# Performance work log

Hardware: AMD Instinct MI355X
Metric: run time of the kernel (lower is better)

The kernel has to match this reference:

```python
import jax, jax.numpy as jnp
import numpy as np
from jax import lax

B, C, T, S = 32, 122, 500, 13
WID, EMB, PROJ = 80, 8, 1024
HID = 768  # (H=1)*(W=96)*(E=8) after CNN
EPS = 1e-5
DN = ('NCHW', 'OIHW', 'NCHW')


def setup_inputs() -> dict:
    key = jax.random.key(0)
    ks = jax.random.split(key, 24)
    f32 = jnp.float32
    def n(k, shape, scale):
        return (jax.random.normal(k, shape, dtype=f32) * scale).astype(f32)
    return {
        'x': jax.random.normal(ks[0], (B, C, T), dtype=f32),
        'subject_ids': jax.random.randint(ks[1], (B,), 0, S, dtype=jnp.int32),
        'W_sub': n(ks[2], (S, T, T), 0.04),      # nn.Linear(500,500) weight per subject
        'b_sub': n(ks[3], (S, T), 0.02),
        'conv1_w': n(ks[4], (WID, 1, 1, 5), 0.3),
        'conv1_b': n(ks[5], (WID,), 0.02),
        'bn1_g': 1.0 + n(ks[6], (WID,), 0.1),
        'bn1_b': n(ks[7], (WID,), 0.1),
        'bn1_m': n(ks[8], (WID,), 0.1),
        'bn1_v': 0.5 + jax.random.uniform(ks[9], (WID,), dtype=f32),
        'conv2_w': n(ks[10], (WID, WID, C, 1), 0.01),
        'conv2_b': n(ks[11], (WID,), 0.02),
        'bn2_g': 1.0 + n(ks[12], (WID,), 0.1),
        'bn2_b': n(ks[13], (WID,), 0.1),
        'bn2_m': n(ks[14], (WID,), 0.1),
        'bn2_v': 0.5 + jax.random.uniform(ks[15], (WID,), dtype=f32),
        'proj_w': n(ks[16], (EMB, WID, 1, 1), 0.1),
        'proj_b': n(ks[17], (EMB,), 0.02),
        'mlp1_w': n(ks[18], (PROJ, HID), 0.03),
        'mlp1_b': n(ks[19], (PROJ,), 0.02),
        'mlp2_w': n(ks[20], (PROJ, PROJ), 0.03),
        'mlp2_b': n(ks[21], (PROJ,), 0.02),
        'ln_g': 1.0 + n(ks[22], (PROJ,), 0.05),
        'ln_b': n(ks[23], (PROJ,), 0.05),
    }


def _bn(h, g, b, m, v):
    # eval-mode BatchNorm2d over channel axis 1
    scale = (g / jnp.sqrt(v + EPS))[None, :, None, None]
    shift = (b - m * g / jnp.sqrt(v + EPS))[None, :, None, None]
    return h * scale + shift


def _forward(x, subject_ids, W_sub, b_sub, conv1_w, conv1_b, bn1_g, bn1_b, bn1_m, bn1_v,
             conv2_w, conv2_b, bn2_g, bn2_b, bn2_m, bn2_v, proj_w, proj_b,
             mlp1_w, mlp1_b, mlp2_w, mlp2_b, ln_g, ln_b):
    # --- per-subject routing: gather each sample's Linear(500,500) and apply ---
    Wg = W_sub[subject_ids]                       # [B,T,T] (out,in)
    bg = b_sub[subject_ids]                       # [B,T]
    out = jnp.einsum('bcs,bts->bct', x, Wg) + bg[:, None, :]
    # --- spatio-temporal CNN (eval mode: dropout = identity) ---
    h = out[:, None, :, :]                        # [B,1,C,T]
    h = lax.conv_general_dilated(h, conv1_w, (1, 1), 'VALID', dimension_numbers=DN)
    h = h + conv1_b[None, :, None, None]          # [B,80,122,496]
    h = lax.reduce_window(h, 0.0, lax.add, (1, 1, 1, 17), (1, 1, 1, 5), 'VALID') / 17.0  # [B,80,122,96]
    h = jax.nn.elu(_bn(h, bn1_g, bn1_b, bn1_m, bn1_v))
    h = lax.conv_general_dilated(h, conv2_w, (1, 1), 'VALID', dimension_numbers=DN)
    h = h + conv2_b[None, :, None, None]          # [B,80,1,96]
    h = jax.nn.elu(_bn(h, bn2_g, bn2_b, bn2_m, bn2_v))
    h = lax.conv_general_dilated(h, proj_w, (1, 1), 'VALID', dimension_numbers=DN)
    h = h + proj_b[None, :, None, None]           # [B,8,1,96]
    z = jnp.transpose(h, (0, 2, 3, 1)).reshape(h.shape[0], -1)  # [B,768]
    # --- MLP projector: Linear -> Residual(GELU+Linear) -> LayerNorm ---
    z1 = z @ mlp1_w.T + mlp1_b                    # [B,1024]
    r = jax.nn.gelu(z1, approximate=False) @ mlp2_w.T + mlp2_b
    y = z1 + r
    mu = jnp.mean(y, axis=-1, keepdims=True)
    var = jnp.var(y, axis=-1, keepdims=True)
    return (y - mu) / jnp.sqrt(var + EPS) * ln_g + ln_b


def reference(x, subject_ids, W_sub, b_sub, conv1_w, conv1_b, bn1_g, bn1_b, bn1_m, bn1_v,
              conv2_w, conv2_b, bn2_g, bn2_b, bn2_m, bn2_v, proj_w, proj_b,
              mlp1_w, mlp1_b, mlp2_w, mlp2_b, ln_g, ln_b):
    return _forward(x, subject_ids, W_sub, b_sub, conv1_w, conv1_b, bn1_g, bn1_b, bn1_m, bn1_v,
                    conv2_w, conv2_b, bn2_g, bn2_b, bn2_m, bn2_v, proj_w, proj_b,
                    mlp1_w, mlp1_b, mlp2_w, mlp2_b, ln_g, ln_b)
```

## Files before the change

### kernel.cpp

```cpp
#include <hip/hip_runtime.h>
#include <math.h>

#define BB 32
#define CC 122
#define TT 500
#define SS 13
#define WID 80
#define EMB 8
#define PROJ 1024
#define HID 768
#define TP 96
#define EPSF 1e-5f
#define KP 9760
#define KSPLIT 16

typedef float f32x4 __attribute__((ext_vector_type(4)));
typedef __bf16 bf16x8 __attribute__((ext_vector_type(8)));
typedef unsigned short u16x8 __attribute__((ext_vector_type(8)));
union BF8 { u16x8 u; bf16x8 b; };

__device__ __forceinline__ unsigned short f2bf(float f) {
    union { float f; unsigned u; } v; v.f = f;
    unsigned r = v.u + 0x7FFFu + ((v.u >> 16) & 1u);
    return (unsigned short)(r >> 16);
}

__device__ __forceinline__ float eluf(float x) {
    return x > 0.f ? x : __expf(x) - 1.f;
}

#define OFF_E    ((size_t)0)
#define OFF_XB   ((size_t)1952000)
#define OFF_W2P  ((size_t)4704512)
#define OFF_PART ((size_t)20086272)
#define OFF_Z    ((size_t)24018432)
#define OFF_Z1   ((size_t)24030720)
#define OFF_G    ((size_t)24063488)
#define OFF_Y    ((size_t)24079872)
#define OFF_W1B  ((size_t)24112640)
#define OFF_W2B  ((size_t)24505856)
#define OFF_WCB  ((size_t)25030144)
#define OFF_B1F  ((size_t)25031424)
#define OFF_SC2  ((size_t)25031504)
#define OFF_SH2  ((size_t)25031584)

#define NPK_X  (2097152)
#define NPK_M1 (786432)
#define NPK_M2 (1048576)
#define NPK_LIN (NPK_X + NPK_M1 + NPK_M2)

__global__ __launch_bounds__(256) void k_pack(const float* __restrict__ x,
                                              const float* __restrict__ conv2_w,
                                              const float* __restrict__ mlp1_w,
                                              const float* __restrict__ mlp2_w,
                                              const float* __restrict__ conv1_w, const float* __restrict__ conv1_b,
                                              const float* __restrict__ g1, const float* __restrict__ b1,
                                              const float* __restrict__ m1, const float* __restrict__ v1,
                                              const float* __restrict__ conv2_b, const float* __restrict__ g2,
                                              const float* __restrict__ b2, const float* __restrict__ m2,
                                              const float* __restrict__ v2,
                                              unsigned short* __restrict__ xb,
                                              unsigned short* __restrict__ w2p,
                                              unsigned short* __restrict__ w1b,
                                              unsigned short* __restrict__ w2b,
                                              unsigned short* __restrict__ wcb, float* __restrict__ bias1f,
                                              float* __restrict__ scale2, float* __restrict__ shift2f) {
    __shared__ unsigned short lt[WID][124];
    int bid = blockIdx.x, tid = threadIdx.x;
    if (bid < WID) {
        if (bid == 0 && tid < WID) {
            int o = tid;
            float s1 = g1[o] * rsqrtf(v1[o] + EPSF);
            float sh1 = b1[o] - m1[o] * s1;
            #pragma unroll
            for (int d = 0; d < 21; d++) {
                int klo = d - 16; if (klo < 0) klo = 0;
                int khi = d;      if (khi > 4) khi = 4;
                float acc = 0.f;
                for (int k = klo; k <= khi; k++) acc += conv1_w[o*5 + k];
                wcb[o*32 + d] = f2bf(acc * s1 * (1.f/17.f));
            }
            #pragma unroll
            for (int d = 21; d < 32; d++) wcb[o*32 + d] = 0;
            bias1f[o] = conv1_b[o] * s1 + sh1;
            float s2 = g2[o] * rsqrtf(v2[o] + EPSF);
            scale2[o] = s2;
            shift2f[o] = conv2_b[o] * s2 + (b2[o] - m2[o] * s2);
        }
        int o = bid;
        const float* src = conv2_w + (size_t)o * (WID * CC);
        for (int i = tid; i < WID * CC; i += 256) {
            int op = i / CC, c = i - op * CC;
            lt[op][c] = f2bf(src[i]);
        }
        __syncthreads();
        unsigned short* dst = w2p + (size_t)o * KP;
        for (int j = tid; j < KP / 8; j += 256) {
            int k0 = j * 8;
            union { unsigned short h[8]; uint4 q; } pk;
            #pragma unroll
            for (int u = 0; u < 8; u++) {
                int k = k0 + u;
                pk.h[u] = lt[k % WID][k / WID];
            }
            *(uint4*)(dst + k0) = pk.q;
        }
        return;
    }
    size_t idx = (size_t)(bid - WID) * 256 + tid;
    if (idx >= (size_t)NPK_LIN) return;
    if (idx < NPK_X) {
        int u = (int)(idx & 7);
        size_t j = idx >> 3;
        int l  = (int)(j & 63); j >>= 6;
        int kk = (int)(j & 15); j >>= 4;
        int sp = (int)(j & 7);
        int b  = (int)(j >> 3);
        int c  = sp * 16 + (l & 15);
        int s  = kk * 32 + (l >> 4) * 8 + u;
        float v = (c < CC && s < TT) ? x[((size_t)b * CC + c) * TT + s] : 0.f;
        xb[idx] = f2bf(v);
    } else if (idx < NPK_X + NPK_M1) {
        size_t j = idx - NPK_X;
        w1b[j] = f2bf(mlp1_w[j]);
    } else {
        size_t j = idx - NPK_X - NPK_M1;
        w2b[j] = f2bf(mlp2_w[j]);
    }
}

__global__ __launch_bounds__(256) void k_einsum(const unsigned short* __restrict__ xb,
                                                const float* __restrict__ W_sub,
                                                const int* __restrict__ sid,
                                                const float* __restrict__ b_sub,
                                                unsigned short* __restrict__ oute) {
    __shared__ unsigned short bt[32 * 520];
    int t0 = blockIdx.x * 32, b = blockIdx.y;
    int s = sid[b];
    int tid = threadIdx.x, w = tid >> 6, lr = tid & 15, lg = (tid >> 4) & 3;
    {
        const float* src = W_sub + (size_t)s * (TT * TT);
        for (int i = tid; i < 2048; i += 256) {
            int row = i >> 6;
            int c0  = (i & 63) << 3;
            int rt  = t0 + row;
            union { unsigned short h[8]; uint4 q; } pk;
            if (rt < TT && c0 + 8 <= TT) {
                const float* p = src + (size_t)rt * TT + c0;
                float4 v0 = *(const float4*)p;
                float4 v1 = *(const float4*)(p + 4);
                pk.h[0] = f2bf(v0.x); pk.h[1] = f2bf(v0.y);
                pk.h[2] = f2bf(v0.z); pk.h[3] = f2bf(v0.w);
                pk.h[4] = f2bf(v1.x); pk.h[5] = f2bf(v1.y);
                pk.h[6] = f2bf(v1.z); pk.h[7] = f2bf(v1.w);
            } else {
                const float* p = src + (size_t)rt * TT;
                #pragma unroll
                for (int j = 0; j < 8; j++)
                    pk.h[j] = (rt < TT && c0 + j < TT) ? f2bf(p[c0 + j]) : (unsigned short)0;
            }
            *(uint4*)(&bt[row * 520 + c0]) = pk.q;
        }
    }
    __syncthreads();
    const unsigned short* A0 = xb + ((size_t)(b * 8 + w * 2) * 16) * 512 + (size_t)(tid & 63) * 8;
    f32x4 acc[2][2] = {};
    for (int kk = 0; kk < 16; kk++) {
        BF8 a0, a1;
        a0.u = *(const u16x8*)(A0 + kk * 512);
        a1.u = *(const u16x8*)(A0 + 16 * 512 + kk * 512);
        #pragma unroll
        for (int nt = 0; nt < 2; nt++) {
            BF8 bf; bf.u = *(const u16x8*)(bt + (nt * 16 + lr) * 520 + kk * 32 + 8 * lg);
            acc[0][nt] = __builtin_amdgcn_mfma_f32_16x16x32_bf16(a0.b, bf.b, acc[0][nt], 0, 0, 0);
            acc[1][nt] = __builtin_amdgcn_mfma_f32_16x16x32_bf16(a1.b, bf.b, acc[1][nt], 0, 0, 0);
        }
    }
    const float* bg = b_sub + (size_t)s * TT;
    #pragma unroll
    for (int nt = 0; nt < 2; nt++) {
        int t = t0 + nt * 16 + lr;
        if (t < TT) {
            float bias = bg[t];
            #pragma unroll
            for (int mt = 0; mt < 2; mt++) {
                int crow = w * 32 + mt * 16 + 4 * lg;
                #pragma unroll
                for (int r = 0; r < 4; r++) {
                    int c = crow + r;
                    if (c < CC) oute[((size_t)b * CC + c) * TT + t] = f2bf(acc[mt][nt][r] + bias);
                }
            }
        }
    }
}

__global__ __launch_bounds__(384) void k_fc(const unsigned short* __restrict__ oute,
                                            const unsigned short* __restrict__ wcb,
                                            const float* __restrict__ b1f,
                                            const unsigned short* __restrict__ w2p,
                                            float* __restrict__ part) {
    __shared__ unsigned short e2[2][512];
    __shared__ unsigned short pt[96][164];
    __shared__ unsigned short aw[WID][168];
    int chunk = blockIdx.x, b = blockIdx.y;
    int tid = threadIdx.x, w = tid >> 6, l = tid & 63, lr = l & 15, lg = l >> 4;
    BF8 af[5]; float4 bf4[5];
    #pragma unroll
    for (int ot = 0; ot < 5; ot++) {
        af[ot].u = *(const u16x8*)(wcb + (ot * 16 + lr) * 32 + 8 * lg);
        bf4[ot] = *(const float4*)(b1f + ot * 16 + 4 * lg);
    }
    f32x4 acc2[5] = {};
    for (int ci = 0; ci < 4; ci++) {
        int cp = chunk * 4 + ci;
        bool live = cp < 61;
        __syncthreads();
        if (live) {
            if (tid < 250) {
                int cc = tid / 125, i = tid % 125;
                ((uint2*)e2[cc])[i] = ((const uint2*)(oute + ((size_t)b * CC + cp * 2 + cc) * TT))[i];
            }
            if (tid >= 232 && tid < 256) {
                int j = tid - 232; int cc = j / 12, i = 500 + (j % 12);
                e2[cc][i] = 0;
            }
            const unsigned short* wsrc = w2p + (size_t)cp * 160;
            for (int i = tid; i < WID * 20; i += 384) {
                int o = i / 20, c8 = i - o * 20;
                *(u16x8*)(&aw[o][c8 * 8]) = *(const u16x8*)(wsrc + (size_t)o * KP + c8 * 8);
            }
        }
        __syncthreads();
        if (live) {
            #pragma unroll
            for (int cc = 0; cc < 2; cc++) {
                int t = w * 16 + lr;
                const unsigned short* ew = e2[cc] + 5 * t + 8 * lg;
                BF8 bfr;
                #pragma unroll
                for (int j = 0; j < 8; j++) bfr.u[j] = ew[j];
                f32x4 fa[5] = {};
                #pragma unroll
                for (int ot = 0; ot < 5; ot++)
                    fa[ot] = __builtin_amdgcn_mfma_f32_16x16x32_bf16(af[ot].b, bfr.b, fa[ot], 0, 0, 0);
                #pragma unroll
                for (int ot = 0; ot < 5; ot++) {
                    union { unsigned short s[4]; uint2 v; } pk;
                    #pragma unroll
                    for (int r = 0; r < 4; r++) pk.s[r] = f2bf(eluf(fa[ot][r] + bf4[ot][r]));
                    *(uint2*)&pt[t][cc * 80 + ot * 16 + 4 * lg] = pk.v;
                }
            }
        }
        __syncthreads();
        if (live) {
            #pragma unroll
            for (int kl = 0; kl < 5; kl++) {
                BF8 bf; bf.u = *(const u16x8*)(&pt[w * 16 + lr][kl * 32 + lg * 8]);
                #pragma unroll
                for (int mt = 0; mt < 5; mt++) {
                    BF8 a; a.u = *(const u16x8*)(&aw[mt * 16 + lr][kl * 32 + lg * 8]);
                    acc2[mt] = __builtin_amdgcn_mfma_f32_16x16x32_bf16(a.b, bf.b, acc2[mt], 0, 0, 0);
                }
            }
        }
    }
    float* pp = part + ((size_t)(chunk * BB + b) * WID) * TP;
    int t = w * 16 + lr;
    #pragma unroll
    for (int mt = 0; mt < 5; mt++) {
        int ob = mt * 16 + 4 * lg;
        #pragma unroll
        for (int r = 0; r < 4; r++)
            pp[(size_t)(ob + r) * TP + t] = acc2[mt][r];
    }
}

__global__ __launch_bounds__(256) void k_redproj(const float* __restrict__ part,
                                                 const float* __restrict__ scale2,
                                                 const float* __restrict__ shift2f,
                                                 const float* __restrict__ pw,
                                                 const float* __restrict__ pb,
                                                 unsigned short* __restrict__ zbf) {
    __shared__ float ly[WID * 12];
    __shared__ float lw[EMB * WID];
    int tq = blockIdx.x, b = blockIdx.y;
    int tid = threadIdx.x;
    int t0 = tq * 12;
    for (int i = tid; i < EMB * WID; i += 256) lw[i] = pw[i];
    if (tid < 240) {
        int o = tid / 3, q = tid % 3;
        const float* pbase = part + (size_t)b * (WID * TP) + o * TP + t0 + 4 * q;
        float4 a = {0.f, 0.f, 0.f, 0.f};
        #pragma unroll
        for (int ks = 0; ks < KSPLIT; ks++) {
            float4 v = *(const float4*)(pbase + (size_t)ks * (BB * WID * TP));
            a.x += v.x; a.y += v.y; a.z += v.z; a.w += v.w;
        }
        float sc = scale2[o], sh = shift2f[o];
        ly[o * 12 + 4 * q + 0] = eluf(a.x * sc + sh);
        ly[o * 12 + 4 * q + 1] = eluf(a.y * sc + sh);
        ly[o * 12 + 4 * q + 2] = eluf(a.z * sc + sh);
        ly[o * 12 + 4 * q + 3] = eluf(a.w * sc + sh);
    }
    __syncthreads();
    if (tid < 12 * EMB) {
        int e = tid & 7, tl = tid >> 3;
        float acc = pb[e];
        #pragma unroll 10
        for (int o = 0; o < WID; o++) acc = fmaf(ly[o * 12 + tl], lw[e * WID + o], acc);
        zbf[(size_t)b * HID + (t0 + tl) * EMB + e] = f2bf(acc);
    }
}

__global__ __launch_bounds__(256) void k_mlp1(const unsigned short* __restrict__ zbf,
                                              const unsigned short* __restrict__ w1b,
                                              const float* __restrict__ bias,
                                              float* __restrict__ z1,
                                              unsigned short* __restrict__ gbf) {
    __shared__ float accb[4][64][4];
    int cu = blockIdx.x >> 1, rh = blockIdx.x & 1;
    int tid = threadIdx.x, w = tid >> 6, l = tid & 63, lr = l & 15, lg = l >> 4;
    int pcol = cu * 16 + lr;
    const unsigned short* wr = w1b + (size_t)pcol * HID + w * 192 + 8 * lg;
    const unsigned short* za = zbf + (size_t)(rh * 16 + lr) * HID + w * 192 + 8 * lg;
    f32x4 acc = {};
    #pragma unroll
    for (int kb = 0; kb < 192; kb += 32) {
        BF8 bf; bf.u = *(const u16x8*)(wr + kb);
        BF8 a;  a.u  = *(const u16x8*)(za + kb);
        acc = __builtin_amdgcn_mfma_f32_16x16x32_bf16(a.b, bf.b, acc, 0, 0, 0);
    }
    #pragma unroll
    for (int r = 0; r < 4; r++) accb[w][l][r] = acc[r];
    __syncthreads();
    if (w == 0) {
        float bs = bias[pcol];
        #pragma unroll
        for (int r = 0; r < 4; r++) {
            int row = rh * 16 + 4 * lg + r;
            float v = bs;
            #pragma unroll
            for (int q = 0; q < 4; q++) v += accb[q][l][r];
            z1[(size_t)row * PROJ + pcol] = v;
            gbf[(size_t)row * PROJ + pcol] = f2bf(0.5f * v * (1.f + erff(v * 0.70710678118654752f)));
        }
    }
}

__global__ __launch_bounds__(256) void k_mlp2(const unsigned short* __restrict__ gbf,
                                              const float* __restrict__ z1,
                                              const unsigned short* __restrict__ w2b,
                                              const float* __restrict__ bias,
                                              float* __restrict__ y) {
    __shared__ float accb[4][64][4];
    int cu = blockIdx.x >> 1, rh = blockIdx.x & 1;
    int tid = threadIdx.x, w = tid >> 6, l = tid & 63, lr = l & 15, lg = l >> 4;
    int pc = cu * 16 + lr;
    const unsigned short* wr = w2b + (size_t)pc * PROJ + w * 256 + 8 * lg;
    const unsigned short* ga = gbf + (size_t)(rh * 16 + lr) * PROJ + w * 256 + 8 * lg;
    f32x4 acc = {};
    #pragma unroll
    for (int kb = 0; kb < 256; kb += 32) {
        BF8 bf; bf.u = *(const u16x8*)(wr + kb);
        BF8 a;  a.u  = *(const u16x8*)(ga + kb);
        acc = __builtin_amdgcn_mfma_f32_16x16x32_bf16(a.b, bf.b, acc, 0, 0, 0);
    }
    #pragma unroll
    for (int r = 0; r < 4; r++) accb[w][l][r] = acc[r];
    __syncthreads();
    if (w == 0) {
        float bs = bias[pc];
        #pragma unroll
        for (int r = 0; r < 4; r++) {
            int row = rh * 16 + 4 * lg + r;
            float v = bs + z1[(size_t)row * PROJ + pc];
            #pragma unroll
            for (int q = 0; q < 4; q++) v += accb[q][l][r];
            y[(size_t)row * PROJ + pc] = v;
        }
    }
}

__global__ __launch_bounds__(256) void k_ln(const float* __restrict__ y,
                                            const float* __restrict__ lg,
                                            const float* __restrict__ lb,
                                            float* __restrict__ out) {
    int b = blockIdx.x, tid = threadIdx.x;
    const float4* yr = (const float4*)(y + (size_t)b * PROJ);
    float4 v = yr[tid];
    float s  = v.x + v.y + v.z + v.w;
    float sq = v.x*v.x + v.y*v.y + v.z*v.z + v.w*v.w;
    #pragma unroll
    for (int off = 32; off > 0; off >>= 1) {
        s  += __shfl_down(s, off);
        sq += __shfl_down(sq, off);
    }
    __shared__ float ss[4], ssq[4];
    int wv = tid >> 6, lane = tid & 63;
    if (lane == 0) { ss[wv] = s; ssq[wv] = sq; }
    __syncthreads();
    __shared__ float smu, sinv;
    if (tid == 0) {
        float Sm = ss[0] + ss[1] + ss[2] + ss[3];
        float Sq = ssq[0] + ssq[1] + ssq[2] + ssq[3];
        float mu = Sm * (1.f / PROJ);
        float var = Sq * (1.f / PROJ) - mu * mu;
        smu = mu;
        sinv = rsqrtf(var + EPSF);
    }
    __syncthreads();
    float mu = smu, inv = sinv;
    float4 g4 = ((const float4*)lg)[tid];
    float4 b4 = ((const float4*)lb)[tid];
    float4 o4;
    o4.x = (v.x - mu) * inv * g4.x + b4.x;
    o4.y = (v.y - mu) * inv * g4.y + b4.y;
    o4.z = (v.z - mu) * inv * g4.z + b4.z;
    o4.w = (v.w - mu) * inv * g4.w + b4.w;
    ((float4*)(out + (size_t)b * PROJ))[tid] = o4;
}

extern "C" void kernel_launch(void* const* d_in, const int* in_sizes, int n_in,
                              void* d_out, int out_size, void* d_ws, size_t ws_size,
                              hipStream_t stream) {
    const float* x        = (const float*)d_in[0];
    const int*   sid      = (const int*)  d_in[1];
    const float* W_sub    = (const float*)d_in[2];
    const float* b_sub    = (const float*)d_in[3];
    const float* conv1_w  = (const float*)d_in[4];
    const float* conv1_b  = (const float*)d_in[5];
    const float* bn1_g    = (const float*)d_in[6];
    const float* bn1_b    = (const float*)d_in[7];
    const float* bn1_m    = (const float*)d_in[8];
    const float* bn1_v    = (const float*)d_in[9];
    const float* conv2_w  = (const float*)d_in[10];
    const float* conv2_b  = (const float*)d_in[11];
    const float* bn2_g    = (const float*)d_in[12];
    const float* bn2_b    = (const float*)d_in[13];
    const float* bn2_m    = (const float*)d_in[14];
    const float* bn2_v    = (const float*)d_in[15];
    const float* proj_w   = (const float*)d_in[16];
    const float* proj_b   = (const float*)d_in[17];
    const float* mlp1_w   = (const float*)d_in[18];
    const float* mlp1_b   = (const float*)d_in[19];
    const float* mlp2_w   = (const float*)d_in[20];
    const float* mlp2_b   = (const float*)d_in[21];
    const float* ln_g     = (const float*)d_in[22];
    const float* ln_b     = (const float*)d_in[23];
    float* out = (float*)d_out;
    float* ws  = (float*)d_ws;

    unsigned short* ws_e   = (unsigned short*)(ws + OFF_E);
    unsigned short* ws_xb  = (unsigned short*)(ws + OFF_XB);
    unsigned short* ws_w2p = (unsigned short*)(ws + OFF_W2P);
    float* ws_part = ws + OFF_PART;
    unsigned short* ws_zbf = (unsigned short*)(ws + OFF_Z);
    float* ws_z1   = ws + OFF_Z1;
    unsigned short* ws_gbf = (unsigned short*)(ws + OFF_G);
    float* ws_y    = ws + OFF_Y;
    unsigned short* ws_w1b = (unsigned short*)(ws + OFF_W1B);
    unsigned short* ws_w2b = (unsigned short*)(ws + OFF_W2B);
    unsigned short* ws_wcb = (unsigned short*)(ws + OFF_WCB);
    float* ws_b1f  = ws + OFF_B1F;
    float* ws_sc2  = ws + OFF_SC2;
    float* ws_sh2  = ws + OFF_SH2;

    hipLaunchKernelGGL(k_pack, dim3(WID + (NPK_LIN + 255) / 256), dim3(256), 0, stream,
                       x, conv2_w, mlp1_w, mlp2_w,
                       conv1_w, conv1_b, bn1_g, bn1_b, bn1_m, bn1_v,
                       conv2_b, bn2_g, bn2_b, bn2_m, bn2_v,
                       ws_xb, ws_w2p, ws_w1b, ws_w2b,
                       ws_wcb, ws_b1f, ws_sc2, ws_sh2);

    hipLaunchKernelGGL(k_einsum, dim3(16, BB), dim3(256), 0, stream,
                       ws_xb, W_sub, sid, b_sub, ws_e);

    hipLaunchKernelGGL(k_fc, dim3(KSPLIT, BB), dim3(384), 0, stream,
                       ws_e, ws_wcb, ws_b1f, ws_w2p, ws_part);

    hipLaunchKernelGGL(k_redproj, dim3(8, BB), dim3(256), 0, stream,
                       ws_part, ws_sc2, ws_sh2, proj_w, proj_b, ws_zbf);

    hipLaunchKernelGGL(k_mlp1, dim3(128), dim3(256), 0, stream,
                       ws_zbf, ws_w1b, mlp1_b, ws_z1, ws_gbf);

    hipLaunchKernelGGL(k_mlp2, dim3(128), dim3(256), 0, stream,
                       ws_gbf, ws_z1, ws_w2b, mlp2_b, ws_y);

    hipLaunchKernelGGL(k_ln, dim3(BB), dim3(256), 0, stream,
                       ws_y, ln_g, ln_b, out);
}
```

Measured before the change: 193.0 us.

## Move weight conversion into einsum launch to overlap with einsum work

Pulls the mlp1/mlp2 bf16 conversion and the conv2 weight repacking out of k_pack and runs them as extra blocks appended to the k_einsum grid. Those blocks need no einsum output, so they can execute alongside the einsum tiles instead of lengthening the serial pack kernel. The mlp copy is also vectorised to 8 elements per thread with float4 loads. The cost is a larger, heterogeneous einsum grid whose copy blocks compete with the einsum tiles for compute units and bandwidth.

```diff
diff --git a/kernel.cpp b/kernel.cpp
--- a/kernel.cpp
+++ b/kernel.cpp
@@ -47,12 +47,11 @@
 #define NPK_X  (2097152)
 #define NPK_M1 (786432)
 #define NPK_M2 (1048576)
-#define NPK_LIN (NPK_X + NPK_M1 + NPK_M2)
+#define M1M2_CHUNKS ((NPK_M1 + NPK_M2) / 8)
+#define NCPY 256
+#define NEIN (512 + NCPY + WID)
 
 __global__ __launch_bounds__(256) void k_pack(const float* __restrict__ x,
-                                              const float* __restrict__ conv2_w,
-                                              const float* __restrict__ mlp1_w,
-                                              const float* __restrict__ mlp2_w,
                                               const float* __restrict__ conv1_w, const float* __restrict__ conv1_b,
                                               const float* __restrict__ g1, const float* __restrict__ b1,
                                               const float* __restrict__ m1, const float* __restrict__ v1,
@@ -60,16 +59,11 @@
                                               const float* __restrict__ b2, const float* __restrict__ m2,
                                               const float* __restrict__ v2,
                                               unsigned short* __restrict__ xb,
-                                              unsigned short* __restrict__ w2p,
-                                              unsigned short* __restrict__ w1b,
-                                              unsigned short* __restrict__ w2b,
                                               unsigned short* __restrict__ wcb, float* __restrict__ bias1f,
                                               float* __restrict__ scale2, float* __restrict__ shift2f) {
-    __shared__ unsigned short lt[WID][124];
-    int bid = blockIdx.x, tid = threadIdx.x;
-    if (bid < WID) {
-        if (bid == 0 && tid < WID) {
-            int o = tid;
+    if (blockIdx.x == 0) {
+        int o = threadIdx.x;
+        if (o < WID) {
             float s1 = g1[o] * rsqrtf(v1[o] + EPSF);
             float sh1 = b1[o] - m1[o] * s1;
             #pragma unroll
@@ -87,57 +81,78 @@
             scale2[o] = s2;
             shift2f[o] = conv2_b[o] * s2 + (b2[o] - m2[o] * s2);
         }
-        int o = bid;
-        const float* src = conv2_w + (size_t)o * (WID * CC);
-        for (int i = tid; i < WID * CC; i += 256) {
-            int op = i / CC, c = i - op * CC;
-            lt[op][c] = f2bf(src[i]);
-        }
-        __syncthreads();
-        unsigned short* dst = w2p + (size_t)o * KP;
-        for (int j = tid; j < KP / 8; j += 256) {
-            int k0 = j * 8;
-            union { unsigned short h[8]; uint4 q; } pk;
-            #pragma unroll
-            for (int u = 0; u < 8; u++) {
-                int k = k0 + u;
-                pk.h[u] = lt[k % WID][k / WID];
-            }
-            *(uint4*)(dst + k0) = pk.q;
-        }
-        return;
-    }
-    size_t idx = (size_t)(bid - WID) * 256 + tid;
-    if (idx >= (size_t)NPK_LIN) return;
-    if (idx < NPK_X) {
-        int u = (int)(idx & 7);
-        size_t j = idx >> 3;
-        int l  = (int)(j & 63); j >>= 6;
-        int kk = (int)(j & 15); j >>= 4;
-        int sp = (int)(j & 7);
-        int b  = (int)(j >> 3);
-        int c  = sp * 16 + (l & 15);
-        int s  = kk * 32 + (l >> 4) * 8 + u;
-        float v = (c < CC && s < TT) ? x[((size_t)b * CC + c) * TT + s] : 0.f;
-        xb[idx] = f2bf(v);
-    } else if (idx < NPK_X + NPK_M1) {
-        size_t j = idx - NPK_X;
-        w1b[j] = f2bf(mlp1_w[j]);
-    } else {
-        size_t j = idx - NPK_X - NPK_M1;
-        w2b[j] = f2bf(mlp2_w[j]);
-    }
+    }
+    size_t idx = (size_t)blockIdx.x * 256 + threadIdx.x;
+    if (idx >= (size_t)NPK_X) return;
+    int u = (int)(idx & 7);
+    size_t j = idx >> 3;
+    int l  = (int)(j & 63); j >>= 6;
+    int kk = (int)(j & 15); j >>= 4;
+    int sp = (int)(j & 7);
+    int b  = (int)(j >> 3);
+    int c  = sp * 16 + (l & 15);
+    int s  = kk * 32 + (l >> 4) * 8 + u;
+    float v = (c < CC && s < TT) ? x[((size_t)b * CC + c) * TT + s] : 0.f;
+    xb[idx] = f2bf(v);
 }
 
 __global__ __launch_bounds__(256) void k_einsum(const unsigned short* __restrict__ xb,
                                                 const float* __restrict__ W_sub,
                                                 const int* __restrict__ sid,
                                                 const float* __restrict__ b_sub,
-                                                unsigned short* __restrict__ oute) {
+                                                const float* __restrict__ mlp1_w,
+                                                const float* __restrict__ mlp2_w,
+                                                const float* __restrict__ conv2_w,
+                                                unsigned short* __restrict__ oute,
+                                                unsigned short* __restrict__ w1b,
+                                                unsigned short* __restrict__ w2b,
+                                                unsigned short* __restrict__ w2p) {
     __shared__ unsigned short bt[32 * 520];
-    int t0 = blockIdx.x * 32, b = blockIdx.y;
+    int bid = blockIdx.x, tid = threadIdx.x;
+    if (bid >= 512) {
+        int cid = bid - 512;
+        if (cid < NCPY) {
+            for (unsigned jj = (unsigned)cid * 256 + tid; jj < (unsigned)M1M2_CHUNKS; jj += NCPY * 256) {
+                unsigned e0 = jj * 8;
+                const float* src;
+                unsigned short* dst;
+                if (e0 < (unsigned)NPK_M1) { src = mlp1_w + e0; dst = w1b + e0; }
+                else { src = mlp2_w + (e0 - NPK_M1); dst = w2b + (e0 - NPK_M1); }
+                float4 v0 = *(const float4*)src;
+                float4 v1 = *(const float4*)(src + 4);
+                union { unsigned short h[8]; uint4 q; } pk;
+                pk.h[0] = f2bf(v0.x); pk.h[1] = f2bf(v0.y);
+                pk.h[2] = f2bf(v0.z); pk.h[3] = f2bf(v0.w);
+                pk.h[4] = f2bf(v1.x); pk.h[5] = f2bf(v1.y);
+                pk.h[6] = f2bf(v1.z); pk.h[7] = f2bf(v1.w);
+                *(uint4*)dst = pk.q;
+            }
+        } else {
+            unsigned short (*lt)[124] = (unsigned short (*)[124])bt;
+            int o = cid - NCPY;
+            const float* src = conv2_w + (size_t)o * (WID * CC);
+            for (int i = tid; i < WID * CC; i += 256) {
+                int op = i / CC, c = i - op * CC;
+                lt[op][c] = f2bf(src[i]);
+            }
+            __syncthreads();
+            unsigned short* dst = w2p + (size_t)o * KP;
+            for (int jj = tid; jj < KP / 8; jj += 256) {
+                int k0 = jj * 8;
+                union { unsigned short h[8]; uint4 q; } pk;
+                #pragma unroll
+                for (int u = 0; u < 8; u++) {
+                    int k = k0 + u;
+                    pk.h[u] = lt[k % WID][k / WID];
+                }
+                *(uint4*)(dst + k0) = pk.q;
+            }
+        }
+        return;
+    }
+    int t0 = (bid & 15) * 32, b = bid >> 4;
     int s = sid[b];
-    int tid = threadIdx.x, w = tid >> 6, lr = tid & 15, lg = (tid >> 4) & 3;
+    int w = tid >> 6, lr = tid & 15, lg = (tid >> 4) & 3;
     {
         const float* src = W_sub + (size_t)s * (TT * TT);
         for (int i = tid; i < 2048; i += 256) {
@@ -156,8 +171,8 @@
             } else {
                 const float* p = src + (size_t)rt * TT;
                 #pragma unroll
-                for (int j = 0; j < 8; j++)
-                    pk.h[j] = (rt < TT && c0 + j < TT) ? f2bf(p[c0 + j]) : (unsigned short)0;
+                for (int jj = 0; jj < 8; jj++)
+                    pk.h[jj] = (rt < TT && c0 + jj < TT) ? f2bf(p[c0 + jj]) : (unsigned short)0;
             }
             *(uint4*)(&bt[row * 520 + c0]) = pk.q;
         }
@@ -467,15 +482,14 @@
     float* ws_sc2  = ws + OFF_SC2;
     float* ws_sh2  = ws + OFF_SH2;
 
-    hipLaunchKernelGGL(k_pack, dim3(WID + (NPK_LIN + 255) / 256), dim3(256), 0, stream,
-                       x, conv2_w, mlp1_w, mlp2_w,
-                       conv1_w, conv1_b, bn1_g, bn1_b, bn1_m, bn1_v,
+    hipLaunchKernelGGL(k_pack, dim3((NPK_X + 255) / 256), dim3(256), 0, stream,
+                       x, conv1_w, conv1_b, bn1_g, bn1_b, bn1_m, bn1_v,
                        conv2_b, bn2_g, bn2_b, bn2_m, bn2_v,
-                       ws_xb, ws_w2p, ws_w1b, ws_w2b,
-                       ws_wcb, ws_b1f, ws_sc2, ws_sh2);
-
-    hipLaunchKernelGGL(k_einsum, dim3(16, BB), dim3(256), 0, stream,
-                       ws_xb, W_sub, sid, b_sub, ws_e);
+                       ws_xb, ws_wcb, ws_b1f, ws_sc2, ws_sh2);
+
+    hipLaunchKernelGGL(k_einsum, dim3(NEIN), dim3(256), 0, stream,
+                       ws_xb, W_sub, sid, b_sub, mlp1_w, mlp2_w, conv2_w,
+                       ws_e, ws_w1b, ws_w2b, ws_w2p);
 
     hipLaunchKernelGGL(k_fc, dim3(KSPLIT, BB), dim3(384), 0, stream,
                        ws_e, ws_wcb, ws_b1f, ws_w2p, ws_part);
```

New measurement: 189.3 us (median of 2 runs). About the same (-1.9%).
